# Performance work log

Measured on AMD Instinct MI355X. Metric: run time of the kernel, lower is better.

The kernel has to match this reference:

```python
import jax, jax.numpy as jnp
import numpy as np

B, N, D, H = 2, 2048, 1024, 16
DH = D // H  # head dim = 64


def setup_inputs() -> dict:
    key = jax.random.key(0)
    k1, k2, k3 = jax.random.split(key, 3)
    x = jax.random.normal(k1, (B, N, D), dtype=jnp.float32)
    # per-head Linear(D, 3*DH): stacked weights (H, D, 3*DH), biases (H, 3*DH)
    W_qkv = jax.random.normal(k2, (H, D, 3 * DH), dtype=jnp.float32) * 0.02
    b_qkv = jnp.zeros((H, 3 * DH), dtype=jnp.float32)
    W_proj = jax.random.normal(k3, (D, D), dtype=jnp.float32) * 0.02
    b_proj = jnp.zeros((D,), dtype=jnp.float32)
    return {"x": x, "W_qkv": W_qkv, "b_qkv": b_qkv, "W_proj": W_proj, "b_proj": b_proj}


def reference(x, W_qkv, b_qkv, W_proj, b_proj):
    b, n, d = x.shape
    h = W_qkv.shape[0]
    dh = W_qkv.shape[2] // 3
    # all heads' kqv projections at once: (B, H, N, 3*DH)
    qkv = jnp.einsum('bnd,hde->bhne', x, W_qkv) + b_qkv[None, :, None, :]
    # original chunks in order k, q, v
    k, q, v = jnp.split(qkv, 3, axis=-1)  # each (B, H, N, DH)
    # scores[b,h,n,m] = q_n . k_m / sqrt(dh)
    scores = jnp.einsum('bhnd,bhmd->bhnm', q, k) / jnp.sqrt(jnp.asarray(dh, x.dtype))
    causal = jnp.tril(jnp.ones((n, n), dtype=bool))
    scores = jnp.where(causal[None, None, :, :], scores, -jnp.inf)
    A = jax.nn.softmax(scores, axis=-1)
    out = jnp.einsum('bhnm,bhmd->bhnd', A, v)
    # concat heads (head-major order matches the torch cat over head list)
    out = out.transpose(0, 2, 1, 3).reshape(b, n, h * dh)
    return out @ W_proj + b_proj
```

## Files before the change

kernel.cpp:

```cpp
#include <hip/hip_runtime.h>
#include <hip/hip_bf16.h>

typedef __hip_bfloat16 HBF;
typedef __bf16 bf16x8 __attribute__((ext_vector_type(8)));
typedef __bf16 bf16x4 __attribute__((ext_vector_type(4)));
typedef float f32x4 __attribute__((ext_vector_type(4)));
typedef float float4v __attribute__((ext_vector_type(4)));

__device__ __forceinline__ float toF(float x) { return x; }
__device__ __forceinline__ float toF(HBF x) { return __bfloat162float(x); }

#define MFMA16(a, b, c) __builtin_amdgcn_mfma_f32_16x16x32_bf16((a), (b), (c), 0, 0, 0)
#define EXP2F(x) __builtin_amdgcn_exp2f(x)
#define QSCALE 0.18033688011112042f
#define MEMFENCE asm volatile("" ::: "memory")

__device__ __forceinline__ void gload_lds16(const HBF* g, HBF* l) {
  __builtin_amdgcn_global_load_lds((const __attribute__((address_space(1))) void*)g,
                                   (__attribute__((address_space(3))) void*)l, 16, 0, 0);
}

__global__ void prep_k(const float* __restrict__ x, HBF* __restrict__ xb,
                       const float* __restrict__ Wqkv, HBF* __restrict__ wqkv_t,
                       const float* __restrict__ Wproj, HBF* __restrict__ wproj_t) {
  const int bid = blockIdx.x, tid = threadIdx.x;
  if (bid < 4096) {
    int i = bid * 256 + tid;
    float4v a = reinterpret_cast<const float4v*>(x)[i];
    HBF o[4] = {__float2bfloat16(a.x), __float2bfloat16(a.y),
                __float2bfloat16(a.z), __float2bfloat16(a.w)};
    *reinterpret_cast<ulonglong1*>(&xb[i * 4]) = *reinterpret_cast<ulonglong1*>(o);
    return;
  }
  __shared__ float tile[32][33];
  const float* in;
  HBF* out;
  int R, C, gx, gy;
  size_t base;
  if (bid < 7168) {
    int t = bid - 4096;
    int gz = t / 192, rem = t % 192;
    gy = rem / 6; gx = rem % 6;
    R = 1024; C = 192;
    base = (size_t)gz * R * C;
    in = Wqkv; out = wqkv_t;
  } else {
    int t = bid - 7168;
    gy = t / 32; gx = t % 32;
    R = 1024; C = 1024;
    base = 0;
    in = Wproj; out = wproj_t;
  }
  int r0 = gy * 32, c0 = gx * 32;
  int tx = tid & 31, ty = tid >> 5;
#pragma unroll
  for (int i = ty; i < 32; i += 8)
    tile[i][tx] = in[base + (size_t)(r0 + i) * C + c0 + tx];
  __syncthreads();
#pragma unroll
  for (int i = ty; i < 32; i += 8)
    out[base + (size_t)(c0 + i) * R + r0 + tx] = __float2bfloat16(tile[tx][i]);
}

__launch_bounds__(512, 4)
__global__ void gemm_qkv_8ph(const HBF* __restrict__ A, const HBF* __restrict__ Bt,
                             const float* __restrict__ bias,
                             HBF* __restrict__ Kout, HBF* __restrict__ Qout,
                             HBF* __restrict__ Vtout) {
  __shared__ __align__(16) HBF As[2][8192];
  __shared__ __align__(16) HBF Bs[2][12288];
  const int tid = threadIdx.x, lane = tid & 63, w = tid >> 6;
  const int lo = lane & 15, g4 = lane >> 4;
  const int wr = w >> 2, wc = w & 3;
  const int s = ((int)blockIdx.x & 7) * 64 + ((int)blockIdx.x >> 3);
  const int bx = s & 15, by = s >> 4;
  const int m0 = by * 128, n0 = bx * 192;
  const int NT = 16;

  f32x4 acc[4][3];
#pragma unroll
  for (int i = 0; i < 4; i++)
#pragma unroll
    for (int j = 0; j < 3; j++) acc[i][j] = (f32x4){0.f, 0.f, 0.f, 0.f};
  bf16x8 af[4][2], bfr[3][2];

  const int rl0 = w * 8 + (lane >> 3);
  const int rl1 = 64 + rl0;
  const int kc0 = (lane & 7) ^ (rl0 & 7);
  const int kc1 = (lane & 7) ^ (rl1 & 7);

  auto stageA = [&](int kt) {
    HBF* base = &As[kt & 1][0];
    gload_lds16(A + (size_t)(m0 + rl0) * 1024 + kt * 64 + kc0 * 8, base + w * 512);
    gload_lds16(A + (size_t)(m0 + rl1) * 1024 + kt * 64 + kc1 * 8, base + 4096 + w * 512);
  };
  auto stageB = [&](int kt, int g) {
    gload_lds16(Bt + (size_t)(n0 + g * 64 + rl0) * 1024 + kt * 64 + kc0 * 8,
                &Bs[kt & 1][g * 4096] + w * 512);
  };
  auto ldA = [&](int bb, int mt, int ks) -> bf16x8 {
    int row = wr * 64 + mt * 16 + lo;
    return *reinterpret_cast<const bf16x8*>(&As[bb][row * 64 + ((ks * 32 + g4 * 8) ^ ((row & 7) * 8))]);
  };
  auto ldB = [&](int bb, int nt, int ks) -> bf16x8 {
    int row = wc * 48 + nt * 16 + lo;
    return *reinterpret_cast<const bf16x8*>(&Bs[bb][row * 64 + ((ks * 32 + g4 * 8) ^ ((row & 7) * 8))]);
  };

  stageA(0); stageB(0, 0); stageB(0, 1); stageB(0, 2);
  stageA(1);
  asm volatile("s_waitcnt vmcnt(2)" ::: "memory");
  __builtin_amdgcn_s_barrier();
  MEMFENCE;

  for (int t = 0; t < NT; ++t) {
    const int bb = t & 1;
#pragma unroll
    for (int mt = 0; mt < 4; ++mt) { af[mt][0] = ldA(bb, mt, 0); af[mt][1] = ldA(bb, mt, 1); }
#pragma unroll
    for (int nt = 0; nt < 2; ++nt) { bfr[nt][0] = ldB(bb, nt, 0); bfr[nt][1] = ldB(bb, nt, 1); }
    if (t + 1 < NT) stageB(t + 1, 0);
    MEMFENCE; __builtin_amdgcn_s_barrier(); MEMFENCE;
    __builtin_amdgcn_s_setprio(1);
#pragma unroll
    for (int mt = 0; mt < 4; ++mt)
#pragma unroll
      for (int nt = 0; nt < 2; ++nt)
#pragma unroll
        for (int ks = 0; ks < 2; ++ks) acc[mt][nt] = MFMA16(af[mt][ks], bfr[nt][ks], acc[mt][nt]);
    __builtin_amdgcn_s_setprio(0);
    MEMFENCE; __builtin_amdgcn_s_barrier(); MEMFENCE;
    bfr[2][0] = ldB(bb, 2, 0); bfr[2][1] = ldB(bb, 2, 1);
    if (t + 1 < NT) { stageB(t + 1, 1); stageB(t + 1, 2); }
    if (t + 2 < NT) stageA(t + 2);
    MEMFENCE; __builtin_amdgcn_s_barrier(); MEMFENCE;
    __builtin_amdgcn_s_setprio(1);
#pragma unroll
    for (int mt = 0; mt < 4; ++mt)
#pragma unroll
      for (int ks = 0; ks < 2; ++ks) acc[mt][2] = MFMA16(af[mt][ks], bfr[2][ks], acc[mt][2]);
    __builtin_amdgcn_s_setprio(0);
    if (t + 2 < NT) {
      asm volatile("s_waitcnt vmcnt(2)" ::: "memory");
    } else {
      asm volatile("s_waitcnt vmcnt(0)" ::: "memory");
    }
    __builtin_amdgcn_s_barrier();
    MEMFENCE;
  }

#pragma unroll
  for (int mt = 0; mt < 4; ++mt) {
    int mrow = m0 + wr * 64 + mt * 16 + g4 * 4;
#pragma unroll
    for (int nt = 0; nt < 3; ++nt) {
      int e = wc * 48 + nt * 16 + lo;
      float bv = bias[bx * 192 + e];
#pragma unroll
      for (int r = 0; r < 4; ++r) {
        int mm = mrow + r;
        int b = mm >> 11, n = mm & 2047;
        float v = acc[mt][nt][r] + bv;
        size_t bh64 = (size_t)(b * 16 + bx);
        if (e < 64)       Kout[(bh64 * 2048 + n) * 64 + e] = __float2bfloat16(v);
        else if (e < 128) Qout[(bh64 * 2048 + n) * 64 + e - 64] = __float2bfloat16(v * QSCALE);
        else              Vtout[(bh64 * 64 + (e - 128)) * 2048 + n] = __float2bfloat16(v);
      }
    }
  }
}

__launch_bounds__(256)
__global__ void gemm_proj_k(const HBF* __restrict__ A, const HBF* __restrict__ Bt,
                            int M, int N, int K, const float* __restrict__ bias,
                            float* __restrict__ Cout) {
  __shared__ __align__(16) HBF As[128 * 64];
  __shared__ __align__(16) HBF Bs[128 * 64];
  const int tid = threadIdx.x;
  const int lane = tid & 63;
  const int w = tid >> 6;
  const int lo = lane & 15, g4 = lane >> 4;
  const int m0 = blockIdx.y * 128, n0 = blockIdx.x * 128;
  const int wr = w >> 1, wc = w & 1;

  const f32x4 zero = {0.f, 0.f, 0.f, 0.f};
  f32x4 acc[4][4];
#pragma unroll
  for (int i = 0; i < 4; i++)
#pragma unroll
    for (int j = 0; j < 4; j++) acc[i][j] = zero;

  for (int k0 = 0; k0 < K; k0 += 64) {
#pragma unroll
    for (int c = 0; c < 4; ++c) {
      int chunk = c * 256 + tid;
      int row = chunk >> 3, kc = (chunk & 7) * 8;
      HBF* ldsA = As + (size_t)(c * 256 + w * 64) * 8;
      HBF* ldsB = Bs + (size_t)(c * 256 + w * 64) * 8;
      gload_lds16(A + (size_t)(m0 + row) * K + k0 + kc, ldsA);
      gload_lds16(Bt + (size_t)(n0 + row) * K + k0 + kc, ldsB);
    }
    __syncthreads();
#pragma unroll
    for (int kk = 0; kk < 2; ++kk) {
      bf16x8 af[4], bfr[4];
#pragma unroll
      for (int i = 0; i < 4; i++)
        af[i] = *reinterpret_cast<const bf16x8*>(As + (size_t)(wr * 64 + i * 16 + lo) * 64 + kk * 32 + g4 * 8);
#pragma unroll
      for (int j = 0; j < 4; j++)
        bfr[j] = *reinterpret_cast<const bf16x8*>(Bs + (size_t)(wc * 64 + j * 16 + lo) * 64 + kk * 32 + g4 * 8);
#pragma unroll
      for (int i = 0; i < 4; i++)
#pragma unroll
        for (int j = 0; j < 4; j++) acc[i][j] = MFMA16(af[i], bfr[j], acc[i][j]);
    }
    __syncthreads();
  }

#pragma unroll
  for (int i = 0; i < 4; i++) {
    int mrow = m0 + wr * 64 + i * 16 + g4 * 4;
#pragma unroll
    for (int j = 0; j < 4; j++) {
      int col = n0 + wc * 64 + j * 16 + lo;
      float bv = bias[col];
#pragma unroll
      for (int r = 0; r < 4; r++)
        Cout[(size_t)(mrow + r) * N + col] = acc[i][j][r] + bv;
    }
  }
}

__launch_bounds__(256, 2)
__global__ void attn_fwd_k(const HBF* __restrict__ Qb, const HBF* __restrict__ Kb,
                           const HBF* __restrict__ Vt, HBF* __restrict__ Ob) {
  __shared__ __align__(16) HBF Ks[2][2][4096];
  __shared__ __align__(16) HBF Vs[2][2][4096];
  __shared__ __align__(16) HBF pLds[4][2048];
  const int tid = threadIdx.x;
  const int lane = tid & 63;
  const int w = tid >> 6;
  const int lo = lane & 15, g4 = lane >> 4;

  const int lin = blockIdx.x;
  const int xcd = lin & 7, c = lin >> 3;
  const int bh = xcd * 4 + (c & 3);
  const int j = 31 - (c >> 2);
  const int b = bh >> 4, h = bh & 15;
  const int qrow0 = j * 64 + w * 16;
  const int nkv = (j + 2) >> 1;

  const HBF* Qp = Qb + (size_t)bh * 2048 * 64;
  const HBF* Kp = Kb + (size_t)bh * 2048 * 64;
  const HBF* Vp = Vt + (size_t)bh * 64 * 2048;

  bf16x8 qf[2];
#pragma unroll
  for (int ds = 0; ds < 2; ds++)
    qf[ds] = *reinterpret_cast<const bf16x8*>(Qp + (size_t)(qrow0 + lo) * 64 + ds * 32 + g4 * 8);

  const f32x4 zero = {0.f, 0.f, 0.f, 0.f};
  f32x4 o[4];
  float m = -1e30f, l = 0.f;
#pragma unroll
  for (int j4 = 0; j4 < 4; j4++) o[j4] = zero;

  const int srow = (lane >> 3) & 7;
  const int sch = lane & 7;
  const int psw = (lo & 7) << 4;

  auto stage = [&](int kv0, int sb) {
#pragma unroll
    for (int sub = 0; sub < 2; sub++)
#pragma unroll
      for (int cc = 0; cc < 2; cc++) {
        int seg = w * 2 + cc;
        int row = seg * 8 + srow;
        gload_lds16(Kp + (size_t)(kv0 + sub * 64 + row) * 64 + ((sch ^ (row & 7)) * 8),
                    &Ks[sb][sub][seg * 512]);
        gload_lds16(Vp + (size_t)row * 2048 + kv0 + sub * 64 + ((sch ^ (row & 7)) * 8),
                    &Vs[sb][sub][seg * 512]);
      }
  };

  stage(0, 0);
  __syncthreads();

  for (int t = 0; t < nkv; ++t) {
    const int kv0 = t * 128;
    const int sb = t & 1;
    if (t + 1 < nkv) stage(kv0 + 128, sb ^ 1);

    f32x4 st[2][4];
#pragma unroll
    for (int sub = 0; sub < 2; sub++)
#pragma unroll
      for (int kt = 0; kt < 4; kt++) {
        int krow = kt * 16 + lo;
        bf16x8 kf0 = *reinterpret_cast<const bf16x8*>(&Ks[sb][sub][krow * 64 + ((g4 ^ (krow & 7)) * 8)]);
        bf16x8 kf1 = *reinterpret_cast<const bf16x8*>(&Ks[sb][sub][krow * 64 + (((4 + g4) ^ (krow & 7)) * 8)]);
        f32x4 z = zero;
        z = MFMA16(kf0, qf[0], z);
        z = MFMA16(kf1, qf[1], z);
        st[sub][kt] = z;
      }

    const int q = qrow0 + lo;
    float pmax = -1e30f;
    if (t == nkv - 1) {
#pragma unroll
      for (int sub = 0; sub < 2; sub++)
#pragma unroll
        for (int kt = 0; kt < 4; kt++)
#pragma unroll
          for (int r = 0; r < 4; r++) {
            int key = kv0 + sub * 64 + kt * 16 + g4 * 4 + r;
            float v = (key <= q) ? st[sub][kt][r] : -1e30f;
            st[sub][kt][r] = v;
            pmax = fmaxf(pmax, v);
          }
    } else {
#pragma unroll
      for (int sub = 0; sub < 2; sub++)
#pragma unroll
        for (int kt = 0; kt < 4; kt++)
#pragma unroll
          for (int r = 0; r < 4; r++) pmax = fmaxf(pmax, st[sub][kt][r]);
    }
    pmax = fmaxf(pmax, __shfl_xor(pmax, 16));
    pmax = fmaxf(pmax, __shfl_xor(pmax, 32));
    if (__any(pmax > m + 11.5f)) {
      float mn = fmaxf(m, pmax);
      float al = EXP2F(m - mn);
      m = mn;
      l *= al;
      float alr[4];
#pragma unroll
      for (int r = 0; r < 4; r++) alr[r] = __shfl(al, g4 * 4 + r);
#pragma unroll
      for (int j4 = 0; j4 < 4; j4++)
#pragma unroll
        for (int r = 0; r < 4; r++) o[j4][r] *= alr[r];
    }
#pragma unroll
    for (int sub = 0; sub < 2; sub++)
#pragma unroll
      for (int kt = 0; kt < 4; kt++)
#pragma unroll
        for (int r = 0; r < 4; r++) {
          float p = EXP2F(st[sub][kt][r] - m);
          st[sub][kt][r] = p;
          l += p;
        }
#pragma unroll
    for (int sub = 0; sub < 2; sub++)
#pragma unroll
      for (int kt = 0; kt < 4; kt++) {
        bf16x4 pk;
#pragma unroll
        for (int r = 0; r < 4; r++) pk[r] = (__bf16)st[sub][kt][r];
        *reinterpret_cast<bf16x4*>(
            &pLds[w][lo * 128 + (((sub * 128 + kt * 32 + g4 * 8) ^ psw) >> 1)]) = pk;
      }
    asm volatile("s_waitcnt lgkmcnt(0)" ::: "memory");
    __builtin_amdgcn_sched_barrier(0);

    bf16x8 pa[4];
#pragma unroll
    for (int ks = 0; ks < 4; ks++)
      pa[ks] = *reinterpret_cast<const bf16x8*>(
          &pLds[w][lo * 128 + (((ks * 64 + g4 * 16) ^ psw) >> 1)]);
#pragma unroll
    for (int j4 = 0; j4 < 4; j4++) {
      int vrow = j4 * 16 + lo;
#pragma unroll
      for (int ks = 0; ks < 4; ks++) {
        bf16x8 vb = *reinterpret_cast<const bf16x8*>(
            &Vs[sb][ks >> 1][vrow * 64 + ((((ks & 1) * 4 + g4) ^ (vrow & 7)) * 8)]);
        o[j4] = MFMA16(pa[ks], vb, o[j4]);
      }
    }
    __syncthreads();
  }

  l += __shfl_xor(l, 16);
  l += __shfl_xor(l, 32);
  float linv = 1.f / l;
  float lr[4];
#pragma unroll
  for (int r = 0; r < 4; r++) lr[r] = __shfl(linv, g4 * 4 + r);
#pragma unroll
  for (int j4 = 0; j4 < 4; j4++)
#pragma unroll
    for (int r = 0; r < 4; r++) {
      int q = qrow0 + g4 * 4 + r;
      Ob[(size_t)(b * 2048 + q) * 1024 + h * 64 + j4 * 16 + lo] =
          __float2bfloat16(o[j4][r] * lr[r]);
    }
}

extern "C" void kernel_launch(void* const* d_in, const int* in_sizes, int n_in,
                              void* d_out, int out_size, void* d_ws, size_t ws_size,
                              hipStream_t stream) {
  const float* x      = (const float*)d_in[0];
  const float* W_qkv  = (const float*)d_in[1];
  const float* b_qkv  = (const float*)d_in[2];
  const float* W_proj = (const float*)d_in[3];
  const float* b_proj = (const float*)d_in[4];
  float* out = (float*)d_out;

  const int B = 2, N = 2048, D = 1024, H = 16, DH = 64;
  const int M = B * N;

  char* ws = (char*)d_ws;
  HBF* xb      = (HBF*)ws; ws += (size_t)M * D * 2;
  HBF* wqkv_t  = (HBF*)ws; ws += (size_t)H * 3 * DH * D * 2;
  HBF* wproj_t = (HBF*)ws; ws += (size_t)D * D * 2;
  HBF* Qb      = (HBF*)ws; ws += (size_t)B * H * N * DH * 2;
  HBF* Kb      = (HBF*)ws; ws += (size_t)B * H * N * DH * 2;
  HBF* Vt      = (HBF*)ws; ws += (size_t)B * H * DH * N * 2;
  HBF* Ob      = (HBF*)ws; ws += (size_t)M * D * 2;

  prep_k<<<8192, 256, 0, stream>>>(x, xb, W_qkv, wqkv_t, W_proj, wproj_t);
  gemm_qkv_8ph<<<512, 512, 0, stream>>>(xb, wqkv_t, b_qkv, Kb, Qb, Vt);
  attn_fwd_k<<<1024, 256, 0, stream>>>(Qb, Kb, Vt, Ob);
  gemm_proj_k<<<dim3(D / 128, M / 128), 256, 0, stream>>>(Ob, wproj_t, M, D, D, b_proj, out);
}
```

Before: 104.9 us.

## Pipeline output projection GEMM with double-buffered swizzled LDS and smaller tiles

Rewrites the output projection GEMM to use 64x128 tiles over 512 blocks, with XCD-aware block remapping. A/B tiles are double-buffered in LDS with an XOR swizzle, and global-to-LDS loads for the next stages are issued during the MFMA phases. Priority hints around the MFMAs and split barriers aim to overlap memory with compute and remove bank conflicts. In exchange it adds more barriers per k-step and hardcodes the problem shape.

Measured after the change: 97.31 us, median of 2. 1.08x faster.

```diff
diff --git a/kernel.cpp b/kernel.cpp
--- a/kernel.cpp
+++ b/kernel.cpp
@@ -170,64 +170,104 @@
   }
 }
 
-__launch_bounds__(256)
+__launch_bounds__(256, 3)
 __global__ void gemm_proj_k(const HBF* __restrict__ A, const HBF* __restrict__ Bt,
-                            int M, int N, int K, const float* __restrict__ bias,
-                            float* __restrict__ Cout) {
-  __shared__ __align__(16) HBF As[128 * 64];
-  __shared__ __align__(16) HBF Bs[128 * 64];
-  const int tid = threadIdx.x;
-  const int lane = tid & 63;
-  const int w = tid >> 6;
+                            const float* __restrict__ bias, float* __restrict__ Cout) {
+  __shared__ __align__(16) HBF As[2][4096];
+  __shared__ __align__(16) HBF Bs[2][8192];
+  const int tid = threadIdx.x, lane = tid & 63, w = tid >> 6;
   const int lo = lane & 15, g4 = lane >> 4;
-  const int m0 = blockIdx.y * 128, n0 = blockIdx.x * 128;
-  const int wr = w >> 1, wc = w & 1;
-
-  const f32x4 zero = {0.f, 0.f, 0.f, 0.f};
-  f32x4 acc[4][4];
-#pragma unroll
-  for (int i = 0; i < 4; i++)
-#pragma unroll
-    for (int j = 0; j < 4; j++) acc[i][j] = zero;
-
-  for (int k0 = 0; k0 < K; k0 += 64) {
-#pragma unroll
-    for (int c = 0; c < 4; ++c) {
-      int chunk = c * 256 + tid;
-      int row = chunk >> 3, kc = (chunk & 7) * 8;
-      HBF* ldsA = As + (size_t)(c * 256 + w * 64) * 8;
-      HBF* ldsB = Bs + (size_t)(c * 256 + w * 64) * 8;
-      gload_lds16(A + (size_t)(m0 + row) * K + k0 + kc, ldsA);
-      gload_lds16(Bt + (size_t)(n0 + row) * K + k0 + kc, ldsB);
-    }
-    __syncthreads();
-#pragma unroll
-    for (int kk = 0; kk < 2; ++kk) {
-      bf16x8 af[4], bfr[4];
-#pragma unroll
-      for (int i = 0; i < 4; i++)
-        af[i] = *reinterpret_cast<const bf16x8*>(As + (size_t)(wr * 64 + i * 16 + lo) * 64 + kk * 32 + g4 * 8);
-#pragma unroll
-      for (int j = 0; j < 4; j++)
-        bfr[j] = *reinterpret_cast<const bf16x8*>(Bs + (size_t)(wc * 64 + j * 16 + lo) * 64 + kk * 32 + g4 * 8);
-#pragma unroll
-      for (int i = 0; i < 4; i++)
-#pragma unroll
-        for (int j = 0; j < 4; j++) acc[i][j] = MFMA16(af[i], bfr[j], acc[i][j]);
-    }
-    __syncthreads();
-  }
-
-#pragma unroll
-  for (int i = 0; i < 4; i++) {
-    int mrow = m0 + wr * 64 + i * 16 + g4 * 4;
-#pragma unroll
-    for (int j = 0; j < 4; j++) {
-      int col = n0 + wc * 64 + j * 16 + lo;
+  const int wrp = w >> 1, wcp = w & 1;
+  const int s = ((int)blockIdx.x & 7) * 64 + ((int)blockIdx.x >> 3);
+  const int bxn = s & 7, by = s >> 3;
+  const int m0 = by * 64, n0 = bxn * 128;
+  const int NT = 16;
+
+  f32x4 acc[2][4];
+#pragma unroll
+  for (int i = 0; i < 2; i++)
+#pragma unroll
+    for (int j = 0; j < 4; j++) acc[i][j] = (f32x4){0.f, 0.f, 0.f, 0.f};
+  bf16x8 af[2][2], bfr[4][2];
+
+  const int rr = tid >> 3;
+  const int ch = tid & 7;
+
+  auto stageA = [&](int kt, int h) {
+    int row = h * 32 + rr;
+    gload_lds16(A + (size_t)(m0 + row) * 1024 + kt * 64 + ((ch ^ (row & 7)) * 8),
+                &As[kt & 1][h * 2048] + w * 512);
+  };
+  auto stageB = [&](int kt, int g) {
+    int row = g * 32 + rr;
+    gload_lds16(Bt + (size_t)(n0 + row) * 1024 + kt * 64 + ((ch ^ (row & 7)) * 8),
+                &Bs[kt & 1][g * 2048] + w * 512);
+  };
+  auto ldA = [&](int bb, int mt, int ks) -> bf16x8 {
+    int row = wrp * 32 + mt * 16 + lo;
+    return *reinterpret_cast<const bf16x8*>(&As[bb][row * 64 + ((ks * 32 + g4 * 8) ^ ((row & 7) * 8))]);
+  };
+  auto ldB = [&](int bb, int nt, int ks) -> bf16x8 {
+    int row = wcp * 64 + nt * 16 + lo;
+    return *reinterpret_cast<const bf16x8*>(&Bs[bb][row * 64 + ((ks * 32 + g4 * 8) ^ ((row & 7) * 8))]);
+  };
+
+  stageA(0, 0); stageA(0, 1);
+  stageB(0, 0); stageB(0, 1); stageB(0, 2); stageB(0, 3);
+  stageA(1, 0); stageA(1, 1);
+  asm volatile("s_waitcnt vmcnt(2)" ::: "memory");
+  __builtin_amdgcn_s_barrier();
+  MEMFENCE;
+
+  for (int t = 0; t < NT; ++t) {
+    const int bb = t & 1;
+#pragma unroll
+    for (int mt = 0; mt < 2; ++mt) { af[mt][0] = ldA(bb, mt, 0); af[mt][1] = ldA(bb, mt, 1); }
+#pragma unroll
+    for (int nt = 0; nt < 2; ++nt) { bfr[nt][0] = ldB(bb, nt, 0); bfr[nt][1] = ldB(bb, nt, 1); }
+    if (t + 1 < NT) { stageB(t + 1, 0); stageB(t + 1, 1); }
+    MEMFENCE; __builtin_amdgcn_s_barrier(); MEMFENCE;
+    __builtin_amdgcn_s_setprio(1);
+#pragma unroll
+    for (int mt = 0; mt < 2; ++mt)
+#pragma unroll
+      for (int nt = 0; nt < 2; ++nt)
+#pragma unroll
+        for (int ks = 0; ks < 2; ++ks) acc[mt][nt] = MFMA16(af[mt][ks], bfr[nt][ks], acc[mt][nt]);
+    __builtin_amdgcn_s_setprio(0);
+    MEMFENCE; __builtin_amdgcn_s_barrier(); MEMFENCE;
+#pragma unroll
+    for (int nt = 2; nt < 4; ++nt) { bfr[nt][0] = ldB(bb, nt, 0); bfr[nt][1] = ldB(bb, nt, 1); }
+    if (t + 1 < NT) { stageB(t + 1, 2); stageB(t + 1, 3); }
+    if (t + 2 < NT) { stageA(t + 2, 0); stageA(t + 2, 1); }
+    MEMFENCE; __builtin_amdgcn_s_barrier(); MEMFENCE;
+    __builtin_amdgcn_s_setprio(1);
+#pragma unroll
+    for (int mt = 0; mt < 2; ++mt)
+#pragma unroll
+      for (int nt = 2; nt < 4; ++nt)
+#pragma unroll
+        for (int ks = 0; ks < 2; ++ks) acc[mt][nt] = MFMA16(af[mt][ks], bfr[nt][ks], acc[mt][nt]);
+    __builtin_amdgcn_s_setprio(0);
+    if (t + 2 < NT) {
+      asm volatile("s_waitcnt vmcnt(2)" ::: "memory");
+    } else {
+      asm volatile("s_waitcnt vmcnt(0)" ::: "memory");
+    }
+    __builtin_amdgcn_s_barrier();
+    MEMFENCE;
+  }
+
+#pragma unroll
+  for (int mt = 0; mt < 2; ++mt) {
+    int mrow = m0 + wrp * 32 + mt * 16 + g4 * 4;
+#pragma unroll
+    for (int nt = 0; nt < 4; ++nt) {
+      int col = n0 + wcp * 64 + nt * 16 + lo;
       float bv = bias[col];
 #pragma unroll
-      for (int r = 0; r < 4; r++)
-        Cout[(size_t)(mrow + r) * N + col] = acc[i][j][r] + bv;
+      for (int r = 0; r < 4; ++r)
+        Cout[(size_t)(mrow + r) * 1024 + col] = acc[mt][nt][r] + bv;
     }
   }
 }
@@ -425,5 +465,5 @@
   prep_k<<<8192, 256, 0, stream>>>(x, xb, W_qkv, wqkv_t, W_proj, wproj_t);
   gemm_qkv_8ph<<<512, 512, 0, stream>>>(xb, wqkv_t, b_qkv, Kb, Qb, Vt);
   attn_fwd_k<<<1024, 256, 0, stream>>>(Qb, Kb, Vt, Ob);
-  gemm_proj_k<<<dim3(D / 128, M / 128), 256, 0, stream>>>(Ob, wproj_t, M, D, D, b_proj, out);
-}
+  gemm_proj_k<<<512, 256, 0, stream>>>(Ob, wproj_t, b_proj, out);
+}
```
